# Optimization experiments

Hardware: AMD Instinct MI355X
Metric: run time of the kernel (lower is better)

The kernel has to match this reference:

```python
import jax, jax.numpy as jnp
import numpy as np
from jax import lax

B, T, D, H, L = 16, 256, 128, 128, 4  # batch, seq, input_size, hidden, num_layers
NUM_CLASSES = 10
EPS = 1e-5


def instancenorm(x):
    # x: [B, T, C]; InstanceNorm1d normalizes over the length dim (T) per (B, C),
    # biased variance, eps=1e-5, no affine.
    m = x.mean(axis=1, keepdims=True)
    v = x.var(axis=1, keepdims=True)
    return (x - m) / jnp.sqrt(v + EPS)


def lstm_stack(x, Wih, Whh, bih, bhh):
    # x: [B, T, I]; Wih/Whh: [L, 4H, I_or_H]; bih/bhh: [L, 4H]. Gate order i,f,g,o.
    batch = x.shape[0]
    hid = Whh.shape[-1]
    out = x
    for l in range(Wih.shape[0]):
        wih, whh, b = Wih[l], Whh[l], bih[l] + bhh[l]
        h0 = jnp.zeros((batch, hid), dtype=x.dtype)
        c0 = jnp.zeros((batch, hid), dtype=x.dtype)
        xs = out.swapaxes(0, 1)  # [T, B, I]

        def step(carry, xt):
            h, c = carry
            g = xt @ wih.T + h @ whh.T + b
            i, f, gg, o = jnp.split(g, 4, axis=-1)
            c_new = jax.nn.sigmoid(f) * c + jax.nn.sigmoid(i) * jnp.tanh(gg)
            h_new = jax.nn.sigmoid(o) * jnp.tanh(c_new)
            return (h_new, c_new), h_new

        _, hs = lax.scan(step, (h0, c0), xs)
        out = hs.swapaxes(0, 1)  # [B, T, H]
    return out


def setup_inputs() -> dict:
    key = jax.random.key(0)
    ks = jax.random.split(key, 16)
    s = 1.0 / np.sqrt(H)
    u = lambda k, shape: jax.random.uniform(k, shape, jnp.float32, -s, s)
    return {
        "x": jax.random.normal(ks[0], (B, T, D), jnp.float32),
        "Wih": u(ks[1], (L, 4 * H, D)),   # input_size == hidden_size so shapes stack
        "Whh": u(ks[2], (L, 4 * H, H)),
        "bih": u(ks[3], (L, 4 * H)),
        "bhh": u(ks[4], (L, 4 * H)),
        "proj_h_w": u(ks[5], (H, H)),
        "proj_h_b": u(ks[6], (H,)),
        "proj_x_w": u(ks[7], (H, D)),
        "proj_x_b": u(ks[8], (H,)),
        "attn_w": u(ks[9], (H,)),
        "fc_w": u(ks[10], (NUM_CLASSES, H)),
        "fc_b": u(ks[11], (NUM_CLASSES,)),
    }


def reference(x, Wih, Whh, bih, bhh, proj_h_w, proj_h_b, proj_x_w, proj_x_b, attn_w, fc_w, fc_b):
    batch, seq_len, input_dim = x.shape
    # normalize(): means/stdev are detached; torch std is unbiased (ddof=1)
    means = lax.stop_gradient(x.mean(axis=(0, 1), keepdims=True))
    stdev = lax.stop_gradient(x.std(axis=(0, 1), ddof=1, keepdims=True) + EPS)
    x = (x - means) / stdev
    x = instancenorm(x)

    lstm_out = lstm_stack(x, Wih, Whh, bih, bhh)   # dropout is identity in eval
    lstm_out = instancenorm(lstm_out)

    ph = lstm_out @ proj_h_w.T + proj_h_b           # [B, T, H]
    px = x @ proj_x_w.T + proj_x_b                  # [B, T, H]
    px = instancenorm(px)

    # additive attention over expanded [B, T, D, H] (values identical across D,
    # matching the original broadcast/expand semantics)
    combined = jnp.tanh(
        jnp.broadcast_to((ph + px)[:, :, None, :], (batch, seq_len, input_dim, ph.shape[-1]))
    )
    logits = jnp.einsum("btdh,h->btd", combined, attn_w)       # [B, T, D]
    alpha = jax.nn.softmax(logits.reshape(batch, -1), axis=1)   # softmax over T*D
    attention_map = alpha.reshape(batch, seq_len, input_dim)

    # classify: context = sum over (T, D) of lstm_out_ex * alpha
    context = jnp.einsum("bth,btd->bh", ph, attention_map)      # [B, H]
    out = context @ fc_w.T + fc_b                               # [B, num_classes]
    return out, attention_map
```

## Files before the change

kernel.cpp:

```cpp
#include <hip/hip_runtime.h>
#include <math.h>
#include <cstddef>

#define B_ 16
#define T_ 256
#define D_ 128
#define H_ 128
#define L_ 4
#define G_ 512
#define NC_ 10
#define EPS_ 1e-5f
#define C_ 16
#define NCHUNK_ (T_ / C_)

#define HROW_ 144
#define HOFF(k) ((k) + (((k) >> 5) << 2))

typedef float f4v __attribute__((ext_vector_type(4)));

#define LOAD_W8(w, base)                                                   \
    asm volatile(                                                          \
        "global_load_dwordx4 %0, %8, off\n\t"                             \
        "global_load_dwordx4 %1, %8, off offset:16\n\t"                   \
        "global_load_dwordx4 %2, %8, off offset:32\n\t"                   \
        "global_load_dwordx4 %3, %8, off offset:48\n\t"                   \
        "global_load_dwordx4 %4, %8, off offset:64\n\t"                   \
        "global_load_dwordx4 %5, %8, off offset:80\n\t"                   \
        "global_load_dwordx4 %6, %8, off offset:96\n\t"                   \
        "global_load_dwordx4 %7, %8, off offset:112\n\t"                  \
        "s_waitcnt vmcnt(0)"                                               \
        : "=&v"(w[0]), "=&v"(w[1]), "=&v"(w[2]), "=&v"(w[3]),              \
          "=&v"(w[4]), "=&v"(w[5]), "=&v"(w[6]), "=&v"(w[7])               \
        : "v"(base)                                                        \
        : "memory")

#define DOT32R(dst_, warr_, hvarr_)                                        \
    {                                                                      \
        float d0_ = 0.f, d1_ = 0.f;                                        \
        _Pragma("unroll")                                                  \
        for (int j_ = 0; j_ < 8; j_++) {                                   \
            d0_ = fmaf(warr_[j_].x, hvarr_[j_].x, d0_);                    \
            d1_ = fmaf(warr_[j_].y, hvarr_[j_].y, d1_);                    \
            d0_ = fmaf(warr_[j_].z, hvarr_[j_].z, d0_);                    \
            d1_ = fmaf(warr_[j_].w, hvarr_[j_].w, d1_);                    \
        }                                                                  \
        dst_ = d0_ + d1_;                                                  \
    }

__device__ __forceinline__ float sigmoid_(float x) {
    x = fminf(fmaxf(x, -30.f), 30.f);
    return 1.f / (1.f + __expf(-x));
}
__device__ __forceinline__ float tanh_(float x) {
    float ax = fminf(fabsf(x), 15.f);
    float e = __expf(2.f * ax);
    float t = 1.f - 2.f / (e + 1.f);
    return copysignf(t, x);
}
__device__ __forceinline__ void wait_ge_(int* p, int v) {
    if (__hip_atomic_load(p, __ATOMIC_RELAXED, __HIP_MEMORY_SCOPE_AGENT) < v) {
        do { __builtin_amdgcn_s_sleep(1); }
        while (__hip_atomic_load(p, __ATOMIC_RELAXED, __HIP_MEMORY_SCOPE_AGENT) < v);
    }
    (void)__hip_atomic_load(p, __ATOMIC_ACQUIRE, __HIP_MEMORY_SCOPE_AGENT);
}

__global__ __launch_bounds__(512) void stats_bd(const float* __restrict__ x,
                                                float* __restrict__ sum_bd,
                                                float* __restrict__ sq_bd) {
    int b = blockIdx.x;
    int tid = threadIdx.x;
    int d = tid & 127, r = tid >> 7;
    const float* xb = x + (size_t)b * T_ * D_;
    float s = 0.f, q = 0.f;
    for (int t = r; t < T_; t += 4) {
        float v = xb[t * D_ + d];
        s += v; q += v * v;
    }
    __shared__ float ls[512], lq[512];
    ls[tid] = s; lq[tid] = q;
    __syncthreads();
    if (r == 0) {
        s = ls[d] + ls[d + 128] + ls[d + 256] + ls[d + 384];
        q = lq[d] + lq[d + 128] + lq[d + 256] + lq[d + 384];
        sum_bd[b * 128 + d] = s;
        sq_bd[b * 128 + d] = q;
    }
}

__global__ __launch_bounds__(128) void stats_norm(const float* __restrict__ sum_bd,
                                                  const float* __restrict__ sq_bd,
                                                  float* __restrict__ mu_bd,
                                                  float* __restrict__ invn) {
    int d = threadIdx.x;
    float s = 0.f, q = 0.f;
    for (int b = 0; b < B_; b++) { s += sum_bd[b * 128 + d]; q += sq_bd[b * 128 + d]; }
    float n = (float)(B_ * T_);
    float m = s / n;
    float varu = (q - n * m * m) / (n - 1.f);
    float sd = sqrtf(fmaxf(varu, 0.f)) + EPS_;
    for (int b = 0; b < B_; b++) {
        float mu = sum_bd[b * 128 + d] * (1.f / T_);
        float varT = sq_bd[b * 128 + d] * (1.f / T_) - mu * mu;
        mu_bd[b * 128 + d] = mu;
        invn[b * 128 + d] = rsqrtf(fmaxf(varT, 0.f) + EPS_ * sd * sd);
    }
}

__global__ __launch_bounds__(256) void gemm_norm_k128(const float* __restrict__ A,
                                                      const float* __restrict__ mu,
                                                      const float* __restrict__ inv,
                                                      const float* __restrict__ Bw,
                                                      const float* __restrict__ b1,
                                                      const float* __restrict__ b2,
                                                      float* __restrict__ C, int N) {
    __shared__ __align__(16) float As[16][64];
    __shared__ __align__(16) float Bs[16][64];
    int tid = threadIdx.x;
    int m0 = blockIdx.x * 64, n0 = blockIdx.y * 64;
    int lr = tid >> 2;
    int lc = (tid & 3) << 2;
    int tm = (tid >> 4) << 2;
    int tn = (tid & 15) << 2;
    float acc[4][4] = {};
    int bidx = (m0 + lr) >> 8;
    const float* Arow = A + (size_t)(m0 + lr) * 128 + lc;
    const float* Brow = Bw + (size_t)(n0 + lr) * 128 + lc;
    const float* mup = mu + bidx * 128 + lc;
    const float* ivp = inv + bidx * 128 + lc;
    for (int kb = 0; kb < 128; kb += 16) {
        float4 av = *(const float4*)(Arow + kb);
        float4 m4 = *(const float4*)(mup + kb);
        float4 i4 = *(const float4*)(ivp + kb);
        av.x = (av.x - m4.x) * i4.x; av.y = (av.y - m4.y) * i4.y;
        av.z = (av.z - m4.z) * i4.z; av.w = (av.w - m4.w) * i4.w;
        float4 bv = *(const float4*)(Brow + kb);
        __syncthreads();
        As[lc + 0][lr] = av.x; As[lc + 1][lr] = av.y; As[lc + 2][lr] = av.z; As[lc + 3][lr] = av.w;
        Bs[lc + 0][lr] = bv.x; Bs[lc + 1][lr] = bv.y; Bs[lc + 2][lr] = bv.z; Bs[lc + 3][lr] = bv.w;
        __syncthreads();
#pragma unroll
        for (int k = 0; k < 16; k++) {
            float4 a4 = *(const float4*)&As[k][tm];
            float4 b4 = *(const float4*)&Bs[k][tn];
            float ar[4] = {a4.x, a4.y, a4.z, a4.w};
            float br[4] = {b4.x, b4.y, b4.z, b4.w};
#pragma unroll
            for (int i = 0; i < 4; i++)
#pragma unroll
                for (int j = 0; j < 4; j++)
                    acc[i][j] = fmaf(ar[i], br[j], acc[i][j]);
        }
    }
#pragma unroll
    for (int i = 0; i < 4; i++) {
        int row = m0 + tm + i;
#pragma unroll
        for (int j = 0; j < 4; j++) {
            int col = n0 + tn + j;
            float bias = b1[col] + (b2 ? b2[col] : 0.f);
            C[(size_t)row * N + col] = acc[i][j] + bias;
        }
    }
}

__global__ __attribute__((amdgpu_waves_per_eu(2, 2))) __launch_bounds__(512)
void scan_pipe5(const float* __restrict__ g0,
                const float* __restrict__ x,
                const float* __restrict__ Wih, const float* __restrict__ Whh,
                const float* __restrict__ bih, const float* __restrict__ bhh,
                const float* __restrict__ proj_x_w, const float* __restrict__ proj_x_b,
                const float* __restrict__ mu_bd, const float* __restrict__ invn,
                float* __restrict__ h_glob,
                float* __restrict__ ring,
                float* __restrict__ px,
                float* __restrict__ mu_px, float* __restrict__ inv_px,
                float* __restrict__ mu_ln, float* __restrict__ inv_ln,
                int* __restrict__ flag_h,
                int* __restrict__ flag_g) {
    const int wg = blockIdx.x;
    const int tid = threadIdx.x;
    __shared__ __align__(16) float shbuf[16 * HROW_];

    if (wg < 64) {
        const int r = tid >> 2, q = tid & 3;
        const int l = wg >> 4, b = wg & 15;
        f4v w0[8], w1[8], w2[8], w3[8];
        const float* wl = Whh + (size_t)l * G_ * 128;
        LOAD_W8(w0, wl + ((size_t)(0 * 128 + r)) * 128 + q * 32);
        LOAD_W8(w1, wl + ((size_t)(1 * 128 + r)) * 128 + q * 32);
        LOAD_W8(w2, wl + ((size_t)(2 * 128 + r)) * 128 + q * 32);
        LOAD_W8(w3, wl + ((size_t)(3 * 128 + r)) * 128 + q * 32);
        float c = 0.f;
        if (tid < HROW_) shbuf[tid] = 0.f;
        const float* g0p = g0 + (size_t)b * T_ * G_;
        const float* rsl = (l > 0) ? ring + ((size_t)(l - 1) * 16 + b) * (4 * C_ * G_) : ring;
        float* hob = h_glob + ((size_t)l * 16 + b) * T_ * 128;
        int* fg = (l > 0) ? flag_g + (l - 1) * 16 + b : flag_g;
        int* fh = flag_h + l * 16 + b;
        float hreg[C_];
        __syncthreads();

        for (int k = 0; k < NCHUNK_; k++) {
            if (l > 0) {
                if (tid == 0) wait_ge_(fg, k + 1);
                __syncthreads();
            }
#pragma unroll
            for (int half = 0; half < 2; half++) {
                float p0[8], p1[8], p2[8], p3[8];
#pragma unroll
                for (int s8 = 0; s8 < 8; s8++) {
                    int s = half * 8 + s8;
                    if (l == 0) {
                        const float* gp = g0p + (size_t)(k * C_ + s) * G_;
                        p0[s8] = gp[r]; p1[s8] = gp[128 + r];
                        p2[s8] = gp[256 + r]; p3[s8] = gp[384 + r];
                    } else {
                        const float* gp = rsl + ((size_t)(k & 3) * C_ + s) * G_;
                        p0[s8] = __hip_atomic_load(gp + r, __ATOMIC_RELAXED, __HIP_MEMORY_SCOPE_AGENT);
                        p1[s8] = __hip_atomic_load(gp + 128 + r, __ATOMIC_RELAXED, __HIP_MEMORY_SCOPE_AGENT);
                        p2[s8] = __hip_atomic_load(gp + 256 + r, __ATOMIC_RELAXED, __HIP_MEMORY_SCOPE_AGENT);
                        p3[s8] = __hip_atomic_load(gp + 384 + r, __ATOMIC_RELAXED, __HIP_MEMORY_SCOPE_AGENT);
                    }
                }
#pragma unroll
                for (int s8 = 0; s8 < 8; s8++) {
                    int s = half * 8 + s8;
                    int t = k * C_ + s;
                    const f4v* hb4 = (const f4v*)(shbuf + (t & 1) * HROW_ + q * 36);
                    f4v hv[8];
#pragma unroll
                    for (int j = 0; j < 8; j++) hv[j] = hb4[j];
                    float zi, zf, zg, zo;
                    DOT32R(zi, w0, hv);
                    DOT32R(zf, w1, hv);
                    DOT32R(zg, w2, hv);
                    DOT32R(zo, w3, hv);
                    zi += __shfl_xor(zi, 1); zi += __shfl_xor(zi, 2);
                    zf += __shfl_xor(zf, 1); zf += __shfl_xor(zf, 2);
                    zg += __shfl_xor(zg, 1); zg += __shfl_xor(zg, 2);
                    zo += __shfl_xor(zo, 1); zo += __shfl_xor(zo, 2);
                    zi += p0[s8]; zf += p1[s8]; zg += p2[s8]; zo += p3[s8];
                    float ai = sigmoid_(zi), af = sigmoid_(zf);
                    float ag = tanh_(zg),    ao = sigmoid_(zo);
                    c = fmaf(af, c, ai * ag);
                    float hn = ao * tanh_(c);
                    if (q == 0) shbuf[((t + 1) & 1) * HROW_ + HOFF(r)] = hn;
                    hreg[s] = hn;
                    __syncthreads();
                }
            }
            if (q == 0) {
#pragma unroll
                for (int s = 0; s < C_; s++)
                    __hip_atomic_store(hob + (size_t)(k * C_ + s) * 128 + r, hreg[s],
                                       __ATOMIC_RELAXED, __HIP_MEMORY_SCOPE_AGENT);
            }
            __syncthreads();
            if (tid == 0) __hip_atomic_store(fh, k + 1, __ATOMIC_RELEASE, __HIP_MEMORY_SCOPE_AGENT);
        }
    } else if (wg < 112) {
        const int r = tid >> 2, q = tid & 3;
        const int li = (wg - 64) >> 4;
        const int l = li + 1, b = (wg - 64) & 15;
        f4v w0[8], w1[8], w2[8], w3[8];
        const float* wl = Wih + (size_t)l * G_ * 128;
        LOAD_W8(w0, wl + ((size_t)(0 * 128 + r)) * 128 + q * 32);
        LOAD_W8(w1, wl + ((size_t)(1 * 128 + r)) * 128 + q * 32);
        LOAD_W8(w2, wl + ((size_t)(2 * 128 + r)) * 128 + q * 32);
        LOAD_W8(w3, wl + ((size_t)(3 * 128 + r)) * 128 + q * 32);
        float bs0 = bih[l * G_ + r] + bhh[l * G_ + r];
        float bs1 = bih[l * G_ + 128 + r] + bhh[l * G_ + 128 + r];
        float bs2 = bih[l * G_ + 256 + r] + bhh[l * G_ + 256 + r];
        float bs3 = bih[l * G_ + 384 + r] + bhh[l * G_ + 384 + r];
        const float* hsrc = h_glob + ((size_t)(l - 1) * 16 + b) * T_ * 128;
        float* rout = ring + ((size_t)li * 16 + b) * (4 * C_ * G_);
        int* fhp = flag_h + (l - 1) * 16 + b;
        int* fhme = flag_h + l * 16 + b;
        int* fgo = flag_g + li * 16 + b;

        for (int k = 0; k < NCHUNK_; k++) {
            if (tid == 0) {
                wait_ge_(fhp, k + 1);
                if (k >= 4) wait_ge_(fhme, k - 3);
            }
            __syncthreads();
#pragma unroll
            for (int i = 0; i < 4; i++) {
                int idx = i * 512 + tid;
                shbuf[(idx >> 7) * HROW_ + HOFF(idx & 127)] =
                    __hip_atomic_load(hsrc + (size_t)k * C_ * 128 + idx,
                                      __ATOMIC_RELAXED, __HIP_MEMORY_SCOPE_AGENT);
            }
            __syncthreads();
#pragma unroll
            for (int s = 0; s < C_; s++) {
                const f4v* hb4 = (const f4v*)(shbuf + s * HROW_ + q * 36);
                f4v hv[8];
#pragma unroll
                for (int j = 0; j < 8; j++) hv[j] = hb4[j];
                float z0, z1, z2, z3;
                DOT32R(z0, w0, hv);
                DOT32R(z1, w1, hv);
                DOT32R(z2, w2, hv);
                DOT32R(z3, w3, hv);
                z0 += __shfl_xor(z0, 1); z0 += __shfl_xor(z0, 2);
                z1 += __shfl_xor(z1, 1); z1 += __shfl_xor(z1, 2);
                z2 += __shfl_xor(z2, 1); z2 += __shfl_xor(z2, 2);
                z3 += __shfl_xor(z3, 1); z3 += __shfl_xor(z3, 2);
                if (q == 0) {
                    float* ro = rout + ((size_t)(k & 3) * C_ + s) * G_;
                    __hip_atomic_store(ro + r, z0 + bs0, __ATOMIC_RELAXED, __HIP_MEMORY_SCOPE_AGENT);
                    __hip_atomic_store(ro + 128 + r, z1 + bs1, __ATOMIC_RELAXED, __HIP_MEMORY_SCOPE_AGENT);
                    __hip_atomic_store(ro + 256 + r, z2 + bs2, __ATOMIC_RELAXED, __HIP_MEMORY_SCOPE_AGENT);
                    __hip_atomic_store(ro + 384 + r, z3 + bs3, __ATOMIC_RELAXED, __HIP_MEMORY_SCOPE_AGENT);
                }
            }
            __syncthreads();
            if (tid == 0) __hip_atomic_store(fgo, k + 1, __ATOMIC_RELEASE, __HIP_MEMORY_SCOPE_AGENT);
        }
    } else if (wg < 128) {
        const int b = wg - 112;
        const int h = tid & 127, tq = tid >> 7;
        f4v w0[8], w1[8], w2[8], w3[8];
        LOAD_W8(w0, proj_x_w + (size_t)h * 128 + 0);
        LOAD_W8(w1, proj_x_w + (size_t)h * 128 + 32);
        LOAD_W8(w2, proj_x_w + (size_t)h * 128 + 64);
        LOAD_W8(w3, proj_x_w + (size_t)h * 128 + 96);
        float bsx = proj_x_b[h];
        float muk = mu_bd[b * 128 + h], ivk = invn[b * 128 + h];
        const float* xb = x + (size_t)b * T_ * 128;
        float* pxb = px + (size_t)b * T_ * 128;
        float sacc = 0.f, qacc = 0.f;

        for (int blk = 0; blk < 16; blk++) {
            int t0 = blk * 16;
            __syncthreads();
#pragma unroll
            for (int j = 0; j < 4; j++) {
                int tt = tq * 4 + j;
                float v = xb[(size_t)(t0 + tt) * 128 + h];
                shbuf[tt * HROW_ + HOFF(h)] = (v - muk) * ivk;
            }
            __syncthreads();
#pragma unroll
            for (int j = 0; j < 4; j++) {
                int tt = tq * 4 + j;
                const float* row = shbuf + tt * HROW_;
                f4v hv[8];
                float p0, p1, p2, p3;
                const f4v* r4 = (const f4v*)(row + 0 * 36);
#pragma unroll
                for (int u = 0; u < 8; u++) hv[u] = r4[u];
                DOT32R(p0, w0, hv);
                r4 = (const f4v*)(row + 1 * 36);
#pragma unroll
                for (int u = 0; u < 8; u++) hv[u] = r4[u];
                DOT32R(p1, w1, hv);
                r4 = (const f4v*)(row + 2 * 36);
#pragma unroll
                for (int u = 0; u < 8; u++) hv[u] = r4[u];
                DOT32R(p2, w2, hv);
                r4 = (const f4v*)(row + 3 * 36);
#pragma unroll
                for (int u = 0; u < 8; u++) hv[u] = r4[u];
                DOT32R(p3, w3, hv);
                float val = (p0 + p1) + (p2 + p3) + bsx;
                pxb[(size_t)(t0 + tt) * 128 + h] = val;
                sacc += val; qacc += val * val;
            }
        }
        __syncthreads();
        shbuf[tq * 128 + h] = sacc;
        shbuf[512 + tq * 128 + h] = qacc;
        __syncthreads();
        if (tq == 0) {
            float s = shbuf[h] + shbuf[128 + h] + shbuf[256 + h] + shbuf[384 + h];
            float qq = shbuf[512 + h] + shbuf[640 + h] + shbuf[768 + h] + shbuf[896 + h];
            float m = s * (1.f / T_);
            float v = qq * (1.f / T_) - m * m;
            mu_px[b * 128 + h] = m;
            inv_px[b * 128 + h] = rsqrtf(fmaxf(v, 0.f) + EPS_);
        }
    } else {
        const int b = wg - 128;
        const int h = tid & 127, st = tid >> 7;
        const float* hsrc = h_glob + ((size_t)3 * 16 + b) * T_ * 128;
        int* f3 = flag_h + 3 * 16 + b;
        float s = 0.f, q = 0.f;
        for (int k = 0; k < NCHUNK_; k++) {
            if (tid == 0) wait_ge_(f3, k + 1);
            __syncthreads();
#pragma unroll
            for (int j = 0; j < 4; j++) {
                int tt = st * 4 + j;
                float v = __hip_atomic_load(hsrc + (size_t)(k * C_ + tt) * 128 + h,
                                            __ATOMIC_RELAXED, __HIP_MEMORY_SCOPE_AGENT);
                s += v; q += v * v;
            }
        }
        shbuf[st * 128 + h] = s;
        shbuf[512 + st * 128 + h] = q;
        __syncthreads();
        if (st == 0) {
            float ss = shbuf[h] + shbuf[128 + h] + shbuf[256 + h] + shbuf[384 + h];
            float qq = shbuf[512 + h] + shbuf[640 + h] + shbuf[768 + h] + shbuf[896 + h];
            float m = ss * (1.f / T_);
            float v = qq * (1.f / T_) - m * m;
            mu_ln[b * 128 + h] = m;
            inv_ln[b * 128 + h] = rsqrtf(fmaxf(v, 0.f) + EPS_);
        }
    }
}

__global__ __launch_bounds__(128) void score_kernel(const float* __restrict__ ph,
                                                    const float* __restrict__ px,
                                                    const float* __restrict__ mu_px,
                                                    const float* __restrict__ inv_px,
                                                    const float* __restrict__ attn_w,
                                                    float* __restrict__ lsc) {
    int bt = blockIdx.x;
    int b = bt >> 8;
    int h = threadIdx.x;
    size_t o = (size_t)bt * 128 + h;
    float v = ph[o] + (px[o] - mu_px[b * 128 + h]) * inv_px[b * 128 + h];
    float sv = tanh_(v) * attn_w[h];
    __shared__ float red[128];
    red[h] = sv;
    __syncthreads();
    for (int off = 64; off > 0; off >>= 1) {
        if (h < off) red[h] += red[h + off];
        __syncthreads();
    }
    if (h == 0) lsc[bt] = red[0];
}

__global__ __launch_bounds__(256) void tail3(const float* __restrict__ lsc,
                                             const float* __restrict__ ph,
                                             const float* __restrict__ fc_w,
                                             const float* __restrict__ fc_b,
                                             float* __restrict__ out,
                                             float* __restrict__ out_att) {
    int b = blockIdx.x;
    int tid = threadIdx.x;
    int h = tid & 127, st = tid >> 7;
    const float* phb = ph + (size_t)b * T_ * H_;
    __shared__ float tmp[256], wsh[256], ls[256];
    float v = lsc[b * 256 + tid];
    tmp[tid] = v; __syncthreads();
    for (int off = 128; off > 0; off >>= 1) { if (tid < off) tmp[tid] = fmaxf(tmp[tid], tmp[tid + off]); __syncthreads(); }
    float mx = tmp[0]; __syncthreads();
    float e = __expf(v - mx);
    tmp[tid] = e; __syncthreads();
    for (int off = 128; off > 0; off >>= 1) { if (tid < off) tmp[tid] += tmp[tid + off]; __syncthreads(); }
    wsh[tid] = e / tmp[0];
    __syncthreads();
    {
        float* ob = out_att + (size_t)b * T_ * D_;
        const float invD = 1.f / (float)D_;
        for (int i = tid; i < T_ * D_; i += 256) ob[i] = wsh[i >> 7] * invD;
    }
    {
        float acc = 0.f;
        for (int t = st; t < T_; t += 2) acc = fmaf(phb[t * 128 + h], wsh[t], acc);
        ls[tid] = acc;
        __syncthreads();
        if (tid < 128) ls[tid] = ls[tid] + ls[tid + 128];
        __syncthreads();
        if (tid < NC_) {
            float s = fc_b[tid];
            const float* fw = fc_w + tid * 128;
            for (int k = 0; k < 128; k++) s = fmaf(ls[k], fw[k], s);
            out[b * NC_ + tid] = s;
        }
    }
}

extern "C" void kernel_launch(void* const* d_in, const int* in_sizes, int n_in,
                              void* d_out, int out_size, void* d_ws, size_t ws_size,
                              hipStream_t stream) {
    const float* x        = (const float*)d_in[0];
    const float* Wih      = (const float*)d_in[1];
    const float* Whh      = (const float*)d_in[2];
    const float* bih      = (const float*)d_in[3];
    const float* bhh      = (const float*)d_in[4];
    const float* proj_h_w = (const float*)d_in[5];
    const float* proj_h_b = (const float*)d_in[6];
    const float* proj_x_w = (const float*)d_in[7];
    const float* proj_x_b = (const float*)d_in[8];
    const float* attn_w   = (const float*)d_in[9];
    const float* fc_w     = (const float*)d_in[10];
    const float* fc_b     = (const float*)d_in[11];
    float* out = (float*)d_out;

    float* ws = (float*)d_ws;
    const size_t NTD = (size_t)B_ * T_ * D_;
    float* h_glob = ws;
    float* g0     = h_glob + 4 * NTD;
    float* ring   = g0 + 4 * NTD;
    float* px     = ring + 3 * NTD;
    float* smalls = px + NTD;
    float* sum_bd = smalls;
    float* sq_bd  = sum_bd + 2048;
    float* mu_bd  = sq_bd + 2048;
    float* invn   = mu_bd + 2048;
    float* mu_ln  = invn + 2048;
    float* inv_ln = mu_ln + 2048;
    float* mu_px  = inv_ln + 2048;
    float* inv_px = mu_px + 2048;
    float* lsc    = inv_px + 2048;
    int*   flags  = (int*)(lsc + 4096);
    int*   flag_h = flags;
    int*   flag_g = flags + 64;
    float* ph = h_glob;
    const float* h3 = h_glob + 3 * NTD;

    hipMemsetAsync((void*)flags, 0, 128 * sizeof(int), stream);

    stats_bd<<<16, 512, 0, stream>>>(x, sum_bd, sq_bd);
    stats_norm<<<1, 128, 0, stream>>>(sum_bd, sq_bd, mu_bd, invn);
    dim3 g1(64, 8);
    gemm_norm_k128<<<g1, 256, 0, stream>>>(x, mu_bd, invn, Wih, bih, bhh, g0, G_);

    scan_pipe5<<<144, 512, 0, stream>>>(g0, x, Wih, Whh, bih, bhh,
                                        proj_x_w, proj_x_b, mu_bd, invn,
                                        h_glob, ring, px, mu_px, inv_px,
                                        mu_ln, inv_ln, flag_h, flag_g);

    dim3 g2(64, 2);
    gemm_norm_k128<<<g2, 256, 0, stream>>>(h3, mu_ln, inv_ln, proj_h_w, proj_h_b,
                                           nullptr, ph, H_);

    score_kernel<<<4096, 128, 0, stream>>>(ph, px, mu_px, inv_px, attn_w, lsc);
    tail3<<<16, 256, 0, stream>>>(lsc, ph, fc_w, fc_b, out, out + B_ * NC_);
}
```

Baseline: 497.8 us.

## Fold layer-0 input projection into pipelined scan and fuse proj_h GEMM with scoring

The standalone layer-0 input-projection GEMM is removed. Sixteen extra producer workgroups in the persistent scan kernel now compute layer-0 gate pre-activations chunk by chunk from normalized x into the ring buffer, so layer 0 overlaps its input projection the same way deeper layers already do. Separately, the proj_h GEMM and the per-(b,t) attention score kernel are merged into one kernel that computes ph, adds the normalized px, applies tanh and dots with attn_w in its epilogue. This removes two launches and a round trip of g0 and ph through memory. In exchange, layer 0 now waits on flag-based handoff and the scan grid grows to 160 workgroups, which could add scheduling pressure.

```diff
diff --git a/kernel.cpp b/kernel.cpp
--- a/kernel.cpp
+++ b/kernel.cpp
@@ -107,66 +107,8 @@
     }
 }
 
-__global__ __launch_bounds__(256) void gemm_norm_k128(const float* __restrict__ A,
-                                                      const float* __restrict__ mu,
-                                                      const float* __restrict__ inv,
-                                                      const float* __restrict__ Bw,
-                                                      const float* __restrict__ b1,
-                                                      const float* __restrict__ b2,
-                                                      float* __restrict__ C, int N) {
-    __shared__ __align__(16) float As[16][64];
-    __shared__ __align__(16) float Bs[16][64];
-    int tid = threadIdx.x;
-    int m0 = blockIdx.x * 64, n0 = blockIdx.y * 64;
-    int lr = tid >> 2;
-    int lc = (tid & 3) << 2;
-    int tm = (tid >> 4) << 2;
-    int tn = (tid & 15) << 2;
-    float acc[4][4] = {};
-    int bidx = (m0 + lr) >> 8;
-    const float* Arow = A + (size_t)(m0 + lr) * 128 + lc;
-    const float* Brow = Bw + (size_t)(n0 + lr) * 128 + lc;
-    const float* mup = mu + bidx * 128 + lc;
-    const float* ivp = inv + bidx * 128 + lc;
-    for (int kb = 0; kb < 128; kb += 16) {
-        float4 av = *(const float4*)(Arow + kb);
-        float4 m4 = *(const float4*)(mup + kb);
-        float4 i4 = *(const float4*)(ivp + kb);
-        av.x = (av.x - m4.x) * i4.x; av.y = (av.y - m4.y) * i4.y;
-        av.z = (av.z - m4.z) * i4.z; av.w = (av.w - m4.w) * i4.w;
-        float4 bv = *(const float4*)(Brow + kb);
-        __syncthreads();
-        As[lc + 0][lr] = av.x; As[lc + 1][lr] = av.y; As[lc + 2][lr] = av.z; As[lc + 3][lr] = av.w;
-        Bs[lc + 0][lr] = bv.x; Bs[lc + 1][lr] = bv.y; Bs[lc + 2][lr] = bv.z; Bs[lc + 3][lr] = bv.w;
-        __syncthreads();
-#pragma unroll
-        for (int k = 0; k < 16; k++) {
-            float4 a4 = *(const float4*)&As[k][tm];
-            float4 b4 = *(const float4*)&Bs[k][tn];
-            float ar[4] = {a4.x, a4.y, a4.z, a4.w};
-            float br[4] = {b4.x, b4.y, b4.z, b4.w};
-#pragma unroll
-            for (int i = 0; i < 4; i++)
-#pragma unroll
-                for (int j = 0; j < 4; j++)
-                    acc[i][j] = fmaf(ar[i], br[j], acc[i][j]);
-        }
-    }
-#pragma unroll
-    for (int i = 0; i < 4; i++) {
-        int row = m0 + tm + i;
-#pragma unroll
-        for (int j = 0; j < 4; j++) {
-            int col = n0 + tn + j;
-            float bias = b1[col] + (b2 ? b2[col] : 0.f);
-            C[(size_t)row * N + col] = acc[i][j] + bias;
-        }
-    }
-}
-
 __global__ __attribute__((amdgpu_waves_per_eu(2, 2))) __launch_bounds__(512)
-void scan_pipe5(const float* __restrict__ g0,
-                const float* __restrict__ x,
+void scan_pipe6(const float* __restrict__ x,
                 const float* __restrict__ Wih, const float* __restrict__ Whh,
                 const float* __restrict__ bih, const float* __restrict__ bhh,
                 const float* __restrict__ proj_x_w, const float* __restrict__ proj_x_b,
@@ -193,36 +135,27 @@
         LOAD_W8(w3, wl + ((size_t)(3 * 128 + r)) * 128 + q * 32);
         float c = 0.f;
         if (tid < HROW_) shbuf[tid] = 0.f;
-        const float* g0p = g0 + (size_t)b * T_ * G_;
-        const float* rsl = (l > 0) ? ring + ((size_t)(l - 1) * 16 + b) * (4 * C_ * G_) : ring;
+        const float* rsl = ring + ((size_t)l * 16 + b) * (4 * C_ * G_);
         float* hob = h_glob + ((size_t)l * 16 + b) * T_ * 128;
-        int* fg = (l > 0) ? flag_g + (l - 1) * 16 + b : flag_g;
+        int* fg = flag_g + l * 16 + b;
         int* fh = flag_h + l * 16 + b;
         float hreg[C_];
         __syncthreads();
 
         for (int k = 0; k < NCHUNK_; k++) {
-            if (l > 0) {
-                if (tid == 0) wait_ge_(fg, k + 1);
-                __syncthreads();
-            }
+            if (tid == 0) wait_ge_(fg, k + 1);
+            __syncthreads();
 #pragma unroll
             for (int half = 0; half < 2; half++) {
                 float p0[8], p1[8], p2[8], p3[8];
 #pragma unroll
                 for (int s8 = 0; s8 < 8; s8++) {
                     int s = half * 8 + s8;
-                    if (l == 0) {
-                        const float* gp = g0p + (size_t)(k * C_ + s) * G_;
-                        p0[s8] = gp[r]; p1[s8] = gp[128 + r];
-                        p2[s8] = gp[256 + r]; p3[s8] = gp[384 + r];
-                    } else {
-                        const float* gp = rsl + ((size_t)(k & 3) * C_ + s) * G_;
-                        p0[s8] = __hip_atomic_load(gp + r, __ATOMIC_RELAXED, __HIP_MEMORY_SCOPE_AGENT);
-                        p1[s8] = __hip_atomic_load(gp + 128 + r, __ATOMIC_RELAXED, __HIP_MEMORY_SCOPE_AGENT);
-                        p2[s8] = __hip_atomic_load(gp + 256 + r, __ATOMIC_RELAXED, __HIP_MEMORY_SCOPE_AGENT);
-                        p3[s8] = __hip_atomic_load(gp + 384 + r, __ATOMIC_RELAXED, __HIP_MEMORY_SCOPE_AGENT);
-                    }
+                    const float* gp = rsl + ((size_t)(k & 3) * C_ + s) * G_;
+                    p0[s8] = __hip_atomic_load(gp + r, __ATOMIC_RELAXED, __HIP_MEMORY_SCOPE_AGENT);
+                    p1[s8] = __hip_atomic_load(gp + 128 + r, __ATOMIC_RELAXED, __HIP_MEMORY_SCOPE_AGENT);
+                    p2[s8] = __hip_atomic_load(gp + 256 + r, __ATOMIC_RELAXED, __HIP_MEMORY_SCOPE_AGENT);
+                    p3[s8] = __hip_atomic_load(gp + 384 + r, __ATOMIC_RELAXED, __HIP_MEMORY_SCOPE_AGENT);
                 }
 #pragma unroll
                 for (int s8 = 0; s8 < 8; s8++) {
@@ -260,10 +193,9 @@
             __syncthreads();
             if (tid == 0) __hip_atomic_store(fh, k + 1, __ATOMIC_RELEASE, __HIP_MEMORY_SCOPE_AGENT);
         }
-    } else if (wg < 112) {
+    } else if (wg < 128) {
         const int r = tid >> 2, q = tid & 3;
-        const int li = (wg - 64) >> 4;
-        const int l = li + 1, b = (wg - 64) & 15;
+        const int l = (wg - 64) >> 4, b = (wg - 64) & 15;
         f4v w0[8], w1[8], w2[8], w3[8];
         const float* wl = Wih + (size_t)l * G_ * 128;
         LOAD_W8(w0, wl + ((size_t)(0 * 128 + r)) * 128 + q * 32);
@@ -274,24 +206,33 @@
         float bs1 = bih[l * G_ + 128 + r] + bhh[l * G_ + 128 + r];
         float bs2 = bih[l * G_ + 256 + r] + bhh[l * G_ + 256 + r];
         float bs3 = bih[l * G_ + 384 + r] + bhh[l * G_ + 384 + r];
-        const float* hsrc = h_glob + ((size_t)(l - 1) * 16 + b) * T_ * 128;
-        float* rout = ring + ((size_t)li * 16 + b) * (4 * C_ * G_);
-        int* fhp = flag_h + (l - 1) * 16 + b;
+        const float* hsrc = (l > 0) ? h_glob + ((size_t)(l - 1) * 16 + b) * T_ * 128
+                                    : x + (size_t)b * T_ * 128;
+        float muk = 0.f, ivk = 1.f;
+        if (l == 0) { muk = mu_bd[b * 128 + (tid & 127)]; ivk = invn[b * 128 + (tid & 127)]; }
+        float* rout = ring + ((size_t)l * 16 + b) * (4 * C_ * G_);
+        int* fhp = (l > 0) ? flag_h + (l - 1) * 16 + b : flag_h;
         int* fhme = flag_h + l * 16 + b;
-        int* fgo = flag_g + li * 16 + b;
+        int* fgo = flag_g + l * 16 + b;
 
         for (int k = 0; k < NCHUNK_; k++) {
             if (tid == 0) {
-                wait_ge_(fhp, k + 1);
+                if (l > 0) wait_ge_(fhp, k + 1);
                 if (k >= 4) wait_ge_(fhme, k - 3);
             }
             __syncthreads();
 #pragma unroll
             for (int i = 0; i < 4; i++) {
                 int idx = i * 512 + tid;
-                shbuf[(idx >> 7) * HROW_ + HOFF(idx & 127)] =
-                    __hip_atomic_load(hsrc + (size_t)k * C_ * 128 + idx,
-                                      __ATOMIC_RELAXED, __HIP_MEMORY_SCOPE_AGENT);
+                float v;
+                if (l == 0) {
+                    v = hsrc[(size_t)k * C_ * 128 + idx];
+                    v = (v - muk) * ivk;
+                } else {
+                    v = __hip_atomic_load(hsrc + (size_t)k * C_ * 128 + idx,
+                                          __ATOMIC_RELAXED, __HIP_MEMORY_SCOPE_AGENT);
+                }
+                shbuf[(idx >> 7) * HROW_ + HOFF(idx & 127)] = v;
             }
             __syncthreads();
 #pragma unroll
@@ -320,8 +261,8 @@
             __syncthreads();
             if (tid == 0) __hip_atomic_store(fgo, k + 1, __ATOMIC_RELEASE, __HIP_MEMORY_SCOPE_AGENT);
         }
-    } else if (wg < 128) {
-        const int b = wg - 112;
+    } else if (wg < 144) {
+        const int b = wg - 128;
         const int h = tid & 127, tq = tid >> 7;
         f4v w0[8], w1[8], w2[8], w3[8];
         LOAD_W8(w0, proj_x_w + (size_t)h * 128 + 0);
@@ -384,7 +325,7 @@
             inv_px[b * 128 + h] = rsqrtf(fmaxf(v, 0.f) + EPS_);
         }
     } else {
-        const int b = wg - 128;
+        const int b = wg - 144;
         const int h = tid & 127, st = tid >> 7;
         const float* hsrc = h_glob + ((size_t)3 * 16 + b) * T_ * 128;
         int* f3 = flag_h + 3 * 16 + b;
@@ -414,26 +355,85 @@
     }
 }
 
-__global__ __launch_bounds__(128) void score_kernel(const float* __restrict__ ph,
-                                                    const float* __restrict__ px,
-                                                    const float* __restrict__ mu_px,
-                                                    const float* __restrict__ inv_px,
-                                                    const float* __restrict__ attn_w,
-                                                    float* __restrict__ lsc) {
-    int bt = blockIdx.x;
-    int b = bt >> 8;
-    int h = threadIdx.x;
-    size_t o = (size_t)bt * 128 + h;
-    float v = ph[o] + (px[o] - mu_px[b * 128 + h]) * inv_px[b * 128 + h];
-    float sv = tanh_(v) * attn_w[h];
-    __shared__ float red[128];
-    red[h] = sv;
+__global__ __launch_bounds__(256) void gemm_score(const float* __restrict__ A,
+                                                  const float* __restrict__ mu,
+                                                  const float* __restrict__ inv,
+                                                  const float* __restrict__ Bw,
+                                                  const float* __restrict__ b1,
+                                                  const float* __restrict__ px,
+                                                  const float* __restrict__ mu_px,
+                                                  const float* __restrict__ inv_px,
+                                                  const float* __restrict__ attn_w,
+                                                  float* __restrict__ ph,
+                                                  float* __restrict__ lsc) {
+    __shared__ __align__(16) float As[16][64];
+    __shared__ __align__(16) float Bs[16][128];
+    __shared__ float red[64][17];
+    int tid = threadIdx.x;
+    int m0 = blockIdx.x * 64;
+    int lr = tid >> 2, lc = (tid & 3) << 2;
+    int lrB = tid >> 1, lcB = (tid & 1) << 3;
+    int tr = tid >> 4, tc = tid & 15;
+    int tm = tr << 2, tn = tc << 3;
+    float acc[4][8] = {};
+    int bidx = (m0 + lr) >> 8;
+    const float* Arow = A + (size_t)(m0 + lr) * 128 + lc;
+    const float* mup = mu + bidx * 128 + lc;
+    const float* ivp = inv + bidx * 128 + lc;
+    const float* Brow = Bw + (size_t)lrB * 128 + lcB;
+    for (int kb = 0; kb < 128; kb += 16) {
+        float4 av = *(const float4*)(Arow + kb);
+        float4 m4 = *(const float4*)(mup + kb);
+        float4 i4 = *(const float4*)(ivp + kb);
+        av.x = (av.x - m4.x) * i4.x; av.y = (av.y - m4.y) * i4.y;
+        av.z = (av.z - m4.z) * i4.z; av.w = (av.w - m4.w) * i4.w;
+        float4 bv0 = *(const float4*)(Brow + kb);
+        float4 bv1 = *(const float4*)(Brow + kb + 4);
+        __syncthreads();
+        As[lc + 0][lr] = av.x; As[lc + 1][lr] = av.y; As[lc + 2][lr] = av.z; As[lc + 3][lr] = av.w;
+        Bs[lcB + 0][lrB] = bv0.x; Bs[lcB + 1][lrB] = bv0.y; Bs[lcB + 2][lrB] = bv0.z; Bs[lcB + 3][lrB] = bv0.w;
+        Bs[lcB + 4][lrB] = bv1.x; Bs[lcB + 5][lrB] = bv1.y; Bs[lcB + 6][lrB] = bv1.z; Bs[lcB + 7][lrB] = bv1.w;
+        __syncthreads();
+#pragma unroll
+        for (int k = 0; k < 16; k++) {
+            float ar[4], br[8];
+#pragma unroll
+            for (int i = 0; i < 4; i++) ar[i] = As[k][tm + i];
+#pragma unroll
+            for (int j = 0; j < 8; j++) br[j] = Bs[k][tn + j];
+#pragma unroll
+            for (int i = 0; i < 4; i++)
+#pragma unroll
+                for (int j = 0; j < 8; j++)
+                    acc[i][j] = fmaf(ar[i], br[j], acc[i][j]);
+        }
+    }
+    float spart[4];
+#pragma unroll
+    for (int i = 0; i < 4; i++) {
+        int row = m0 + tm + i;
+        int bb = row >> 8;
+        float sp = 0.f;
+#pragma unroll
+        for (int j = 0; j < 8; j++) {
+            int col = tn + j;
+            float val = acc[i][j] + b1[col];
+            ph[(size_t)row * 128 + col] = val;
+            float inx = (px[(size_t)row * 128 + col] - mu_px[bb * 128 + col]) * inv_px[bb * 128 + col];
+            sp = fmaf(tanh_(val + inx), attn_w[col], sp);
+        }
+        spart[i] = sp;
+    }
     __syncthreads();
-    for (int off = 64; off > 0; off >>= 1) {
-        if (h < off) red[h] += red[h + off];
-        __syncthreads();
-    }
-    if (h == 0) lsc[bt] = red[0];
+#pragma unroll
+    for (int i = 0; i < 4; i++) red[tm + i][tc] = spart[i];
+    __syncthreads();
+    if (tid < 64) {
+        float s = 0.f;
+#pragma unroll
+        for (int j = 0; j < 16; j++) s += red[tid][j];
+        lsc[m0 + tid] = s;
+    }
 }
 
 __global__ __launch_bounds__(256) void tail3(const float* __restrict__ lsc,
@@ -497,9 +497,8 @@
     float* ws = (float*)d_ws;
     const size_t NTD = (size_t)B_ * T_ * D_;
     float* h_glob = ws;
-    float* g0     = h_glob + 4 * NTD;
-    float* ring   = g0 + 4 * NTD;
-    float* px     = ring + 3 * NTD;
+    float* ring   = h_glob + 4 * NTD;
+    float* px     = ring + 4 * NTD;
     float* smalls = px + NTD;
     float* sum_bd = smalls;
     float* sq_bd  = sum_bd + 2048;
@@ -520,18 +519,14 @@
 
     stats_bd<<<16, 512, 0, stream>>>(x, sum_bd, sq_bd);
     stats_norm<<<1, 128, 0, stream>>>(sum_bd, sq_bd, mu_bd, invn);
-    dim3 g1(64, 8);
-    gemm_norm_k128<<<g1, 256, 0, stream>>>(x, mu_bd, invn, Wih, bih, bhh, g0, G_);
-
-    scan_pipe5<<<144, 512, 0, stream>>>(g0, x, Wih, Whh, bih, bhh,
+
+    scan_pipe6<<<160, 512, 0, stream>>>(x, Wih, Whh, bih, bhh,
                                         proj_x_w, proj_x_b, mu_bd, invn,
                                         h_glob, ring, px, mu_px, inv_px,
                                         mu_ln, inv_ln, flag_h, flag_g);
 
-    dim3 g2(64, 2);
-    gemm_norm_k128<<<g2, 256, 0, stream>>>(h3, mu_ln, inv_ln, proj_h_w, proj_h_b,
-                                           nullptr, ph, H_);
-
-    score_kernel<<<4096, 128, 0, stream>>>(ph, px, mu_px, inv_px, attn_w, lsc);
+    gemm_score<<<64, 256, 0, stream>>>(h3, mu_ln, inv_ln, proj_h_w, proj_h_b,
+                                       px, mu_px, inv_px, attn_w, ph, lsc);
+
     tail3<<<16, 256, 0, stream>>>(lsc, ph, fc_w, fc_b, out, out + B_ * NC_);
 }
```

Measured after the change: 493.3 us. No clear change (-0.9%).
